# Kernel optimization log

Hardware: AMD Instinct MI355X
Metric: run time of the kernel (lower is better)

The kernel has to match this reference:

```python
import jax, jax.numpy as jnp
import numpy as np
import math

# Config (matches init_kwargs)
H, SQK, PQK, SV, PV = 12, 16, 4, 16, 8
C1, C2 = 384, 128
NR, NA = 512, 256
N = NR + NA
WC = math.sqrt(2.0 / (9.0 * PQK))
WL = math.sqrt(1.0 / 3.0)


def quat_to_rot(q):
    # q: [..., 4] (w, x, y, z); normalize then build rotation matrix [..., 3, 3]
    q = q / jnp.linalg.norm(q, axis=-1, keepdims=True)
    w, x, y, z = q[..., 0], q[..., 1], q[..., 2], q[..., 3]
    return jnp.stack([
        jnp.stack([1 - 2 * (y * y + z * z), 2 * (x * y - w * z), 2 * (x * z + w * y)], -1),
        jnp.stack([2 * (x * y + w * z), 1 - 2 * (x * x + z * z), 2 * (y * z - w * x)], -1),
        jnp.stack([2 * (x * z - w * y), 2 * (y * z + w * x), 1 - 2 * (x * x + y * y)], -1),
    ], -2)


def setup_inputs() -> dict:
    key = jax.random.key(0)
    ks = jax.random.split(key, 16)
    s = 0.02
    return {
        'rec_1d': jax.random.normal(ks[0], (1, NR, C1), jnp.float32),
        'lig_1d': jax.random.normal(ks[1], (1, NA, C1), jnp.float32),
        'rep_2d': jax.random.normal(ks[2], (1, N, N, C2), jnp.float32),
        'rec_T': jax.random.normal(ks[3], (1, NR, 7), jnp.float32),
        'lig_T': jax.random.normal(ks[4], (1, NA, 7), jnp.float32),
        'rec_w1d': jax.random.normal(ks[5], (C1, (2 * SQK + SV) * H), jnp.float32) * s,
        'rec_wpt': jax.random.normal(ks[6], (C1, (2 * PQK + PV) * H * 3), jnp.float32) * s,
        'lig_w1d': jax.random.normal(ks[7], (C1, (2 * SQK + SV) * H), jnp.float32) * s,
        'lig_wpt': jax.random.normal(ks[8], (C1, (2 * PQK + PV) * H * 3), jnp.float32) * s,
        'rr_w': jax.random.normal(ks[9], (C2, H), jnp.float32) * s,
        'll_w': jax.random.normal(ks[10], (C2, H), jnp.float32) * s,
        'rl_w': jax.random.normal(ks[11], (C2, H), jnp.float32) * s,
        'lr_w': jax.random.normal(ks[12], (C2, H), jnp.float32) * s,
        'final_w': jax.random.normal(ks[13], (H * (C2 + SV + 4 * PV), C1), jnp.float32) * s,
        'final_b': jnp.zeros((C1,), jnp.float32),
    }


def reference(rec_1d, lig_1d, rep_2d, rec_T, lig_T, rec_w1d, rec_wpt, lig_w1d, lig_wpt,
              rr_w, ll_w, rl_w, lr_w, final_w, final_b):
    B = rec_1d.shape[0]

    def scalar_kqv(x, w, n):
        kqv = (x @ w).reshape(B, n, H, 2 * SQK + SV)
        return kqv[..., :SQK], kqv[..., SQK:2 * SQK], kqv[..., 2 * SQK:]

    rec_k1, rec_q1, rec_v1 = scalar_kqv(rec_1d, rec_w1d, NR)
    lig_k1, lig_q1, lig_v1 = scalar_kqv(lig_1d, lig_w1d, NA)

    # 2d pair biases per block: [B, i, j, H]
    rr = rep_2d[:, :NR, :NR] @ rr_w
    ll = rep_2d[:, NR:, NR:] @ ll_w
    rl = rep_2d[:, :NR, NR:] @ rl_w
    lr = rep_2d[:, NR:, :NR] @ lr_w

    def point_kqv(x, w, T, n):
        R = quat_to_rot(T[..., :4])          # [B, n, 3, 3]
        t = T[..., 4:]                        # [B, n, 3]
        local = (x @ w).reshape(B, n, 3, H * (2 * PQK + PV))
        glob = jnp.einsum('bnij,bnjd->bnid', R, local) + t[..., None]
        glob = glob.reshape(B, n, 3, H, 2 * PQK + PV)
        return glob[..., :PQK], glob[..., PQK:2 * PQK], glob[..., 2 * PQK:], R, t

    rec_kp, rec_qp, rec_vp, rec_R, rec_t = point_kqv(rec_1d, rec_wpt, rec_T, NR)
    lig_kp, lig_qp, lig_vp, lig_R, lig_t = point_kqv(lig_1d, lig_wpt, lig_T, NA)

    q_point = jnp.concatenate([rec_qp, lig_qp], axis=1)  # [B, N, 3, H, PQK]
    k_point = jnp.concatenate([rec_kp, lig_kp], axis=1)

    # squared distances summed over xyz and points -> [B, N, N, H]
    diff = q_point[:, :, None] - k_point[:, None, :]     # [B, N, N, 3, H, PQK]
    d2 = jnp.sum(jnp.square(diff), axis=3).sum(axis=-1)
    aff = -WC * d2

    bias = jnp.concatenate([
        jnp.concatenate([rr, rl], axis=2),
        jnp.concatenate([lr, ll], axis=2),
    ], axis=1)
    aff = aff + bias

    q1 = jnp.concatenate([rec_q1, lig_q1], axis=1)
    k1 = jnp.concatenate([rec_k1, lig_k1], axis=1)
    aff = aff + (WL / math.sqrt(SQK)) * jnp.einsum('bihc,bjhc->bijh', q1, k1)

    weights = jax.nn.softmax(aff, axis=2)  # [B, N, N, H]

    # 2d aggregation: [B, N, H, C2]
    o_2d = jnp.einsum('bijh,bijc->bihc', weights, rep_2d).reshape(B, N, H * C2)

    # scalar-v term: faithful to source (v_1d.unsqueeze(2) broadcasts over j,
    # so it reduces to v_1d * sum_j weights)
    v_1d = jnp.concatenate([rec_v1, lig_v1], axis=1)     # [B, N, H, SV]
    o_1d = (v_1d * jnp.sum(weights, axis=2)[..., None]).reshape(B, N, H * SV)

    # point-v aggregation in global frame: [B, N, 3, PV, H]
    v_point = jnp.concatenate([rec_vp, lig_vp], axis=1)  # [B, N, 3, H, PV]
    out_global = jnp.einsum('bijh,bjdhp->bidph', weights, v_point)

    def invert(glob, R, t):
        return jnp.einsum('bnji,bnjph->bniph', R, glob - t[..., None, None])

    out_local = jnp.concatenate([
        invert(out_global[:, :NR], rec_R, rec_t),
        invert(out_global[:, NR:], lig_R, lig_t),
    ], axis=1)                                           # [B, N, 3, PV, H]
    out_local = jnp.transpose(out_local, (0, 1, 3, 4, 2))  # [B, N, PV, H, 3]
    o_pt = out_local.reshape(B, N, PV * H * 3)
    o_norm = jnp.sqrt(jnp.sum(jnp.square(out_local), axis=-1)).reshape(B, N, PV * H)

    feat = jnp.concatenate([o_2d, o_1d, o_pt, o_norm], axis=-1)
    return feat @ final_w + final_b
```

## Files before the change

kernel.cpp:

```cpp
#include <hip/hip_runtime.h>
#include <math.h>

#define H_   12
#define NRR  512
#define N_   768
#define C1_  384
#define C2_  128
static __device__ __constant__ float WC_  = 0.2357022603955158f;
static __device__ __constant__ float SC1_ = 0.14433756729740646f;

#define OFF_Q1     0
#define OFF_QP     147456
#define OFF_V1     258048
#define OFF_VP     405504
#define OFF_R      626688
#define OFF_T      633600
#define OFF_KHAT   635904
#define OFF_WFRAG  930816
#define OFF_QKF    934912
#define OFF_MUSED  10372096
#define OFF_MSFIN  10519552
#define OFF_W      10544128
#define OFF_FEAT   17622016
#define OFF_PART   19244032

typedef __attribute__((ext_vector_type(8))) short short8_m;
typedef __attribute__((ext_vector_type(4))) float f32x4_m;

__device__ __forceinline__ ushort f2bf(float f) {
  uint u = __float_as_uint(f);
  uint r = (u + 0x7fffu + ((u >> 16) & 1u)) >> 16;
  return (ushort)r;
}
__device__ __forceinline__ float bf2f(ushort v) {
  return __uint_as_float(((uint)v) << 16);
}

__global__ __launch_bounds__(192) void proj_kernel(
    const float* __restrict__ rec_1d, const float* __restrict__ lig_1d,
    const float* __restrict__ rec_T,  const float* __restrict__ lig_T,
    const float* __restrict__ rec_w1d, const float* __restrict__ rec_wpt,
    const float* __restrict__ lig_w1d, const float* __restrict__ lig_wpt,
    float* __restrict__ ws) {
  const int tok0 = blockIdx.x * 4;
  const int tid  = threadIdx.x;
  __shared__ float xs[4][384];
  __shared__ float loc[4][576];
  __shared__ float Rs[4][9];
  __shared__ float tts[4][3];

  for (int r = 0; r < 4; ++r) {
    int n = tok0 + r;
    const float* x = (n < NRR) ? rec_1d + n * C1_ : lig_1d + (n - NRR) * C1_;
    for (int k = tid; k < C1_; k += 192) xs[r][k] = x[k];
  }
  if (tid < 4) {
    int n = tok0 + tid;
    const float* T = (n < NRR) ? rec_T + n * 7 : lig_T + (n - NRR) * 7;
    float qw = T[0], qx = T[1], qy = T[2], qz = T[3];
    float inv = 1.0f / sqrtf(qw*qw + qx*qx + qy*qy + qz*qz);
    qw *= inv; qx *= inv; qy *= inv; qz *= inv;
    Rs[tid][0] = 1.f - 2.f*(qy*qy + qz*qz);
    Rs[tid][1] = 2.f*(qx*qy - qw*qz);
    Rs[tid][2] = 2.f*(qx*qz + qw*qy);
    Rs[tid][3] = 2.f*(qx*qy + qw*qz);
    Rs[tid][4] = 1.f - 2.f*(qx*qx + qz*qz);
    Rs[tid][5] = 2.f*(qy*qz - qw*qx);
    Rs[tid][6] = 2.f*(qx*qz - qw*qy);
    Rs[tid][7] = 2.f*(qy*qz + qw*qx);
    Rs[tid][8] = 1.f - 2.f*(qx*qx + qy*qy);
    tts[tid][0] = T[4]; tts[tid][1] = T[5]; tts[tid][2] = T[6];
    float* Rg = ws + OFF_R + n * 9;
    #pragma unroll
    for (int k = 0; k < 9; ++k) Rg[k] = Rs[tid][k];
    float* tg = ws + OFF_T + n * 3;
    tg[0] = T[4]; tg[1] = T[5]; tg[2] = T[6];
  }
  __syncthreads();

  const float* w1 = (tok0 < NRR) ? rec_w1d : lig_w1d;
  const float* w2 = (tok0 < NRR) ? rec_wpt : lig_wpt;
  for (int cc = 0; cc < 3; ++cc) {
    int c = tid + cc * 192;
    float a0=0,a1=0,a2=0,a3=0,b0=0,b1=0,b2=0,b3=0;
    for (int k = 0; k < C1_; ++k) {
      float wv = w1[k * 576 + c];
      float wp = w2[k * 576 + c];
      float x0 = xs[0][k], x1 = xs[1][k], x2 = xs[2][k], x3 = xs[3][k];
      a0 += x0*wv; a1 += x1*wv; a2 += x2*wv; a3 += x3*wv;
      b0 += x0*wp; b1 += x1*wp; b2 += x2*wp; b3 += x3*wp;
    }
    loc[0][c]=b0; loc[1][c]=b1; loc[2][c]=b2; loc[3][c]=b3;
    int h = c / 48, e = c % 48;
    float av[4] = {a0,a1,a2,a3};
    for (int r = 0; r < 4; ++r) {
      int n = tok0 + r;
      if (e < 16)      ws[OFF_KHAT + ((size_t)h*N_ + n)*32 + e] = av[r];
      else if (e < 32) ws[OFF_Q1 + n*192 + h*16 + (e-16)]       = av[r];
      else             ws[OFF_V1 + n*192 + h*16 + (e-32)]       = av[r];
    }
  }
  __syncthreads();

  {
    int cp = tid;
    int h = cp >> 4, e = cp & 15;
    for (int r = 0; r < 4; ++r) {
      int n = tok0 + r;
      float g[3];
      #pragma unroll
      for (int d = 0; d < 3; ++d)
        g[d] = Rs[r][d*3+0]*loc[r][cp] + Rs[r][d*3+1]*loc[r][192+cp]
             + Rs[r][d*3+2]*loc[r][384+cp] + tts[r][d];
      if (e < 4) {
        #pragma unroll
        for (int d = 0; d < 3; ++d)
          ws[OFF_KHAT + ((size_t)h*N_ + n)*32 + 16 + e*3 + d] = g[d];
      } else if (e < 8) {
        #pragma unroll
        for (int d = 0; d < 3; ++d) ws[OFF_QP + n*144 + h*12 + (e-4)*3 + d] = g[d];
      } else {
        #pragma unroll
        for (int d = 0; d < 3; ++d) ws[OFF_VP + n*288 + d*96 + h*8 + (e-8)] = g[d];
      }
    }
  }
}

__global__ __launch_bounds__(256) void wfrag_kernel(
    const float* __restrict__ rr_w, const float* __restrict__ rl_w,
    const float* __restrict__ lr_w, const float* __restrict__ ll_w,
    float* __restrict__ ws) {
  ushort* wf = (ushort*)(ws + OFF_WFRAG);
  const float* mats[4] = { rr_w, rl_w, lr_w, ll_w };
  for (int idx = threadIdx.x; idx < 8192; idx += 256) {
    int mat = idx >> 11;
    int r   = idx & 2047;
    int ks  = r >> 9;
    int r2  = r & 511;
    int l   = r2 >> 3;
    int e   = r2 & 7;
    int n   = l & 15;
    int k   = ks*32 + (l>>4)*8 + e;
    float v = (n < 12) ? mats[mat][k*12 + n] : 0.f;
    wf[idx] = f2bf(v);
  }
}

__global__ __launch_bounds__(256) void qk_kernel(float* __restrict__ ws) {
  const int b = blockIdx.x;
  const int i = b / 12, tile = b % 12;
  const int t = threadIdx.x;
  const int l = t & 63, w = t >> 6;
  __shared__ float q1s[12][16];
  __shared__ float qps[12][12];
  if (t < 192) q1s[t >> 4][t & 15] = ws[OFF_Q1 + i*192 + t];
  if (t < 144) qps[t / 12][t % 12] = ws[OFF_QP + i*144 + t];
  __syncthreads();
  const int h = l & 15, jq = l >> 4;
  float val[4] = {0.f, 0.f, 0.f, 0.f};
  if (h < 12) {
    #pragma unroll
    for (int rr = 0; rr < 4; ++rr) {
      int j = tile*64 + w*16 + jq*4 + rr;
      const float* kf = ws + OFF_KHAT + ((size_t)h*N_ + j)*32;
      float kv[28];
      #pragma unroll
      for (int c = 0; c < 28; c += 4) *(float4*)&kv[c] = *(const float4*)(kf + c);
      float s = 0.f;
      #pragma unroll
      for (int c = 0; c < 16; ++c) s += q1s[h][c] * kv[c];
      float d2 = 0.f;
      #pragma unroll
      for (int d = 0; d < 12; ++d) { float df = qps[h][d] - kv[16+d]; d2 += df*df; }
      val[rr] = SC1_*s - WC_*d2;
    }
  }
  float4 o; o.x = val[0]; o.y = val[1]; o.z = val[2]; o.w = val[3];
  *(float4*)(ws + OFF_QKF + ((size_t)b*4 + w)*256 + l*4) = o;
}

__global__ __launch_bounds__(256) void flash_kernel(
    const float* __restrict__ rep, float* __restrict__ ws) {
  const int i = blockIdx.x;
  const int t = threadIdx.x;
  const int lane = t & 63, wv = t >> 6;
  __shared__ ushort A[64 * 128];
  __shared__ ushort e_l[64 * 16];
  __shared__ float mt[64], est[64], fact[16], mrun[16], srun[16];

  const short8_m* wf = (const short8_m*)(ws + OFF_WFRAG);
  const int m0 = (i < NRR) ? 0 : 2, m1 = (i < NRR) ? 1 : 3;
  short8_m bf0[4], bf1[4];
  #pragma unroll
  for (int ks = 0; ks < 4; ++ks) {
    bf0[ks] = wf[(m0*4 + ks)*64 + lane];
    bf1[ks] = wf[(m1*4 + ks)*64 + lane];
  }
  if (t < 16) { mrun[t] = -1e30f; srun[t] = 0.f; }
  float acc[48];
  #pragma unroll
  for (int k = 0; k < 48; ++k) acc[k] = 0.f;

  const int cq = t & 31, jgr = t >> 5;
  const int hh = lane & 15, jq = lane >> 4;
  const int rowA = wv*16 + hh;
  __syncthreads();

  for (int tile = 0; tile < 12; ++tile) {
    const float* src = rep + ((size_t)i*N_ + tile*64) * C2_;
    #pragma unroll
    for (int k = 0; k < 8; ++k) {
      int j = jgr + k*8;
      float4 v = *(const float4*)(src + j*C2_ + cq*4);
      uint2 p;
      p.x = (uint)f2bf(v.x) | ((uint)f2bf(v.y) << 16);
      p.y = (uint)f2bf(v.z) | ((uint)f2bf(v.w) << 16);
      int slot = (cq >> 1) ^ (j & 7);
      *(uint2*)((char*)A + j*256 + slot*16 + (cq & 1)*8) = p;
    }
    __syncthreads();

    f32x4_m c4 = {0.f, 0.f, 0.f, 0.f};
    #pragma unroll
    for (int ks = 0; ks < 4; ++ks) {
      int slot = (ks*4 + jq) ^ (rowA & 7);
      short8_m a = *(const short8_m*)((const char*)A + rowA*256 + slot*16);
      c4 = __builtin_amdgcn_mfma_f32_16x16x32_bf16(
          a, (tile < 8) ? bf0[ks] : bf1[ks], c4, 0, 0, 0);
    }
    float4 qk4 = *(const float4*)(ws + OFF_QKF +
        (((size_t)i*12 + tile)*4 + wv)*256 + lane*4);
    float aff0 = c4[0] + qk4.x, aff1 = c4[1] + qk4.y;
    float aff2 = c4[2] + qk4.z, aff3 = c4[3] + qk4.w;

    float ml = fmaxf(fmaxf(aff0, aff1), fmaxf(aff2, aff3));
    ml = fmaxf(ml, __shfl_xor(ml, 16));
    ml = fmaxf(ml, __shfl_xor(ml, 32));
    if (jq == 0) mt[wv*16 + hh] = ml;
    __syncthreads();
    if (t < 12) {
      float m4 = fmaxf(fmaxf(mt[t], mt[16+t]), fmaxf(mt[32+t], mt[48+t]));
      float mn = fmaxf(mrun[t], m4);
      fact[t]  = __expf(mrun[t] - mn);
      mrun[t]  = mn;
      ws[OFF_MUSED + (size_t)i*192 + tile*16 + t] = mn;
    }
    __syncthreads();

    const bool valid = (hh < 12);
    float mh = valid ? mrun[hh] : 0.f;
    float e0 = valid ? __expf(aff0 - mh) : 0.f;
    float e1 = valid ? __expf(aff1 - mh) : 0.f;
    float e2 = valid ? __expf(aff2 - mh) : 0.f;
    float e3 = valid ? __expf(aff3 - mh) : 0.f;
    if (valid) {
      int jb = wv*16 + jq*4;
      e_l[(jb+0)*16 + hh] = f2bf(e0);
      e_l[(jb+1)*16 + hh] = f2bf(e1);
      e_l[(jb+2)*16 + hh] = f2bf(e2);
      e_l[(jb+3)*16 + hh] = f2bf(e3);
    }
    float es = e0 + e1 + e2 + e3;
    es += __shfl_xor(es, 16);
    es += __shfl_xor(es, 32);
    if (jq == 0) est[wv*16 + hh] = es;
    __syncthreads();
    if (t < 12)
      srun[t] = srun[t]*fact[t] + (est[t] + est[16+t] + est[32+t] + est[48+t]);

    float fc[12];
    #pragma unroll
    for (int h = 0; h < 12; ++h) fc[h] = fact[h];
    #pragma unroll
    for (int h = 0; h < 12; ++h) {
      acc[h*4+0] *= fc[h]; acc[h*4+1] *= fc[h];
      acc[h*4+2] *= fc[h]; acc[h*4+3] *= fc[h];
    }
    #pragma unroll
    for (int k = 0; k < 8; ++k) {
      int j = jgr + k*8;
      const char* ep = (const char*)e_l + j*32;
      uint4 u4 = *(const uint4*)ep;
      uint2 u2 = *(const uint2*)(ep + 16);
      float ef[12];
      ef[0] = __uint_as_float(u4.x << 16); ef[1] = __uint_as_float(u4.x & 0xffff0000u);
      ef[2] = __uint_as_float(u4.y << 16); ef[3] = __uint_as_float(u4.y & 0xffff0000u);
      ef[4] = __uint_as_float(u4.z << 16); ef[5] = __uint_as_float(u4.z & 0xffff0000u);
      ef[6] = __uint_as_float(u4.w << 16); ef[7] = __uint_as_float(u4.w & 0xffff0000u);
      ef[8] = __uint_as_float(u2.x << 16); ef[9] = __uint_as_float(u2.x & 0xffff0000u);
      ef[10] = __uint_as_float(u2.y << 16); ef[11] = __uint_as_float(u2.y & 0xffff0000u);
      int slot = (cq >> 1) ^ (j & 7);
      uint2 av = *(const uint2*)((const char*)A + j*256 + slot*16 + (cq & 1)*8);
      float af[4];
      af[0] = __uint_as_float(av.x << 16); af[1] = __uint_as_float(av.x & 0xffff0000u);
      af[2] = __uint_as_float(av.y << 16); af[3] = __uint_as_float(av.y & 0xffff0000u);
      #pragma unroll
      for (int h = 0; h < 12; ++h) {
        acc[h*4+0] += ef[h]*af[0];
        acc[h*4+1] += ef[h]*af[1];
        acc[h*4+2] += ef[h]*af[2];
        acc[h*4+3] += ef[h]*af[3];
      }
    }
    #pragma unroll
    for (int k = 0; k < 3; ++k) {
      int h = wv + k*4;
      ws[OFF_W + (size_t)i*9216 + h*768 + tile*64 + lane] =
          bf2f(e_l[lane*16 + h]);
    }
    __syncthreads();
  }

  if (t < 12) {
    ws[OFF_MSFIN + i*32 + t]      = mrun[t];
    ws[OFF_MSFIN + i*32 + 16 + t] = srun[t];
  }
  #pragma unroll
  for (int k = 0; k < 48; ++k) acc[k] += __shfl_xor(acc[k], 32);
  float* scr = (float*)A;
  __syncthreads();
  if (wv >= 2 && lane < 32) {
    float* dst = scr + (wv-2)*1536 + lane*48;
    #pragma unroll
    for (int k = 0; k < 48; ++k) dst[k] = acc[k];
  }
  __syncthreads();
  if (wv < 2 && lane < 32) {
    const float* s2 = scr + wv*1536 + lane*48;
    #pragma unroll
    for (int k = 0; k < 48; ++k) acc[k] += s2[k];
  }
  __syncthreads();
  if (wv == 1 && lane < 32) {
    float* dst = scr + lane*48;
    #pragma unroll
    for (int k = 0; k < 48; ++k) dst[k] = acc[k];
  }
  __syncthreads();
  if (wv == 0 && lane < 32) {
    const float* s2 = scr + lane*48;
    #pragma unroll
    for (int k = 0; k < 48; ++k) acc[k] += s2[k];
    float* feat = ws + OFF_FEAT + (size_t)i*2112;
    #pragma unroll
    for (int h = 0; h < 12; ++h) {
      float inv = 1.0f / srun[h];
      float4 r;
      r.x = acc[h*4+0]*inv; r.y = acc[h*4+1]*inv;
      r.z = acc[h*4+2]*inv; r.w = acc[h*4+3]*inv;
      *(float4*)&feat[h*128 + lane*4] = r;
    }
  }
}

__global__ __launch_bounds__(320) void opoint_kernel(
    const float* __restrict__ ws_w, const float* __restrict__ vp,
    const float* __restrict__ R, const float* __restrict__ tvec,
    const float* __restrict__ v1, const float* __restrict__ mused,
    const float* __restrict__ msfin, float* __restrict__ feat) {
  const int i = blockIdx.x;
  const int tid = threadIdx.x;
  __shared__ float wl[H_ * N_];
  __shared__ float cf[144];
  __shared__ float og[288];
  __shared__ float ol[288];
  if (tid < 144) {
    int h = tid / 12, tl = tid % 12;
    float sfin = msfin[i*32 + 16 + h];
    cf[tid] = __expf(mused[(size_t)i*192 + tl*16 + h] - msfin[i*32 + h]) / sfin;
  }
  __syncthreads();
  for (int k = tid; k < H_*N_; k += 320) {
    int h = k / 768, j = k - h*768;
    wl[k] = ws_w[(size_t)i*9216 + k] * cf[h*12 + (j >> 6)];
  }
  __syncthreads();
  if (tid < 288) {
    int d = tid / 96, hh = (tid % 96) / 8;
    float acc = 0.f;
    for (int j = 0; j < N_; ++j) acc += wl[hh*N_ + j] * vp[(size_t)j*288 + tid];
    og[tid] = acc - tvec[i*3 + d];
  }
  if (tid < 192) feat[(size_t)i*2112 + 1536 + tid] = v1[(size_t)i*192 + tid];
  __syncthreads();
  if (tid < 288) {
    int i3 = tid / 96, rem = tid % 96, hh = rem / 8, p = rem % 8;
    float o = R[i*9 + 0*3 + i3] * og[0*96 + rem]
            + R[i*9 + 1*3 + i3] * og[1*96 + rem]
            + R[i*9 + 2*3 + i3] * og[2*96 + rem];
    ol[tid] = o;
    feat[(size_t)i*2112 + 1728 + p*36 + hh*3 + i3] = o;
  }
  __syncthreads();
  if (tid < 96) {
    int hh = tid / 8, p = tid % 8;
    float a = ol[0*96 + tid], b = ol[1*96 + tid], c = ol[2*96 + tid];
    feat[(size_t)i*2112 + 2016 + p*12 + hh] = sqrtf(a*a + b*b + c*c);
  }
}

__global__ __launch_bounds__(384) void final1_kernel(
    const float* __restrict__ ws, const float* __restrict__ fw,
    float* __restrict__ part) {
  const int i0 = blockIdx.x * 4;
  const int ks = blockIdx.y;
  const int o  = threadIdx.x;
  const int k0 = ks * 1056;
  __shared__ float fl[4 * 1056];
  const float* feat = ws + OFF_FEAT;
  for (int idx = o; idx < 1056; idx += 384) {
    int r = idx / 264, f4 = idx % 264;
    *(float4*)&fl[r*1056 + f4*4] =
        *(const float4*)(feat + (size_t)(i0+r)*2112 + k0 + f4*4);
  }
  __syncthreads();
  float a0=0,a1=0,a2=0,a3=0;
  for (int f4 = 0; f4 < 264; ++f4) {
    int f = k0 + f4*4;
    float w0 = fw[(size_t)(f+0)*384 + o];
    float w1 = fw[(size_t)(f+1)*384 + o];
    float w2 = fw[(size_t)(f+2)*384 + o];
    float w3 = fw[(size_t)(f+3)*384 + o];
    float4 f0 = *(const float4*)&fl[0*1056 + f4*4];
    float4 f1 = *(const float4*)&fl[1*1056 + f4*4];
    float4 f2 = *(const float4*)&fl[2*1056 + f4*4];
    float4 f3 = *(const float4*)&fl[3*1056 + f4*4];
    a0 += f0.x*w0 + f0.y*w1 + f0.z*w2 + f0.w*w3;
    a1 += f1.x*w0 + f1.y*w1 + f1.z*w2 + f1.w*w3;
    a2 += f2.x*w0 + f2.y*w1 + f2.z*w2 + f2.w*w3;
    a3 += f3.x*w0 + f3.y*w1 + f3.z*w2 + f3.w*w3;
  }
  part[((size_t)ks*N_ + i0+0)*384 + o] = a0;
  part[((size_t)ks*N_ + i0+1)*384 + o] = a1;
  part[((size_t)ks*N_ + i0+2)*384 + o] = a2;
  part[((size_t)ks*N_ + i0+3)*384 + o] = a3;
}

__global__ __launch_bounds__(256) void final2_kernel(
    const float* __restrict__ part, const float* __restrict__ fb,
    float* __restrict__ out) {
  int idx = blockIdx.x * 256 + threadIdx.x;
  int col = idx % 384;
  out[idx] = part[idx] + part[294912 + idx] + fb[col];
}

extern "C" void kernel_launch(void* const* d_in, const int* in_sizes, int n_in,
                              void* d_out, int out_size, void* d_ws, size_t ws_size,
                              hipStream_t stream) {
  const float* rec_1d  = (const float*)d_in[0];
  const float* lig_1d  = (const float*)d_in[1];
  const float* rep_2d  = (const float*)d_in[2];
  const float* rec_T   = (const float*)d_in[3];
  const float* lig_T   = (const float*)d_in[4];
  const float* rec_w1d = (const float*)d_in[5];
  const float* rec_wpt = (const float*)d_in[6];
  const float* lig_w1d = (const float*)d_in[7];
  const float* lig_wpt = (const float*)d_in[8];
  const float* rr_w    = (const float*)d_in[9];
  const float* ll_w    = (const float*)d_in[10];
  const float* rl_w    = (const float*)d_in[11];
  const float* lr_w    = (const float*)d_in[12];
  const float* final_w = (const float*)d_in[13];
  const float* final_b = (const float*)d_in[14];
  float* ws  = (float*)d_ws;
  float* out = (float*)d_out;

  proj_kernel<<<192, 192, 0, stream>>>(rec_1d, lig_1d, rec_T, lig_T,
                                       rec_w1d, rec_wpt, lig_w1d, lig_wpt, ws);
  wfrag_kernel<<<1, 256, 0, stream>>>(rr_w, rl_w, lr_w, ll_w, ws);
  qk_kernel<<<N_*12, 256, 0, stream>>>(ws);
  flash_kernel<<<N_, 256, 0, stream>>>(rep_2d, ws);
  opoint_kernel<<<N_, 320, 0, stream>>>(ws + OFF_W, ws + OFF_VP, ws + OFF_R,
                                        ws + OFF_T, ws + OFF_V1, ws + OFF_MUSED,
                                        ws + OFF_MSFIN, ws + OFF_FEAT);
  final1_kernel<<<dim3(N_/4, 2), 384, 0, stream>>>(ws, final_w, ws + OFF_PART);
  final2_kernel<<<1152, 256, 0, stream>>>(ws + OFF_PART, final_b, out);
}
```

Baseline: 986.6 us.

## Split flash attention over key tiles, drop online max, double-buffer rep tiles

The flash kernel now launches three blocks per query row, each covering four of the twelve 64-wide key tiles, and writes partial outputs and exp-sums. A new o2dfin kernel combines the partials and normalises. The running-max rescaling is removed, so exponentials are taken directly on the raw logits. A double-buffered LDS tile with register prefetch of the next rep_2d tile and lighter raw barriers are meant to overlap global loads with compute and cut synchronisation. The cost is an extra kernel and partial-buffer traffic, and large logits could overflow exp because they are no longer shifted by the max.

```diff
diff --git a/kernel.cpp b/kernel.cpp
--- a/kernel.cpp
+++ b/kernel.cpp
@@ -6,6 +6,8 @@
 #define N_   768
 #define C1_  384
 #define C2_  128
+#define SPLIT 3
+#define TPB  4
 static __device__ __constant__ float WC_  = 0.2357022603955158f;
 static __device__ __constant__ float SC1_ = 0.14433756729740646f;
 
@@ -18,11 +20,12 @@
 #define OFF_KHAT   635904
 #define OFF_WFRAG  930816
 #define OFF_QKF    934912
-#define OFF_MUSED  10372096
-#define OFF_MSFIN  10519552
-#define OFF_W      10544128
-#define OFF_FEAT   17622016
-#define OFF_PART   19244032
+#define OFF_SSP    10372096
+#define OFF_SSUM   10408960
+#define OFF_O2DP   10421248
+#define OFF_W      13960192
+#define OFF_FEAT   21038080
+#define OFF_PART   22660096
 
 typedef __attribute__((ext_vector_type(8))) short short8_m;
 typedef __attribute__((ext_vector_type(4))) float f32x4_m;
@@ -35,6 +38,12 @@
 __device__ __forceinline__ float bf2f(ushort v) {
   return __uint_as_float(((uint)v) << 16);
 }
+
+#define BARRAW() do {                                        \
+    asm volatile("s_waitcnt lgkmcnt(0)" ::: "memory");       \
+    __builtin_amdgcn_s_barrier();                            \
+    __builtin_amdgcn_sched_barrier(0);                       \
+  } while (0)
 
 __global__ __launch_bounds__(192) void proj_kernel(
     const float* __restrict__ rec_1d, const float* __restrict__ lig_1d,
@@ -182,101 +191,85 @@
 
 __global__ __launch_bounds__(256) void flash_kernel(
     const float* __restrict__ rep, float* __restrict__ ws) {
-  const int i = blockIdx.x;
+  const int b = blockIdx.x;
+  const int i = b / SPLIT, sp = b % SPLIT;
+  const int t0 = sp * TPB;
   const int t = threadIdx.x;
   const int lane = t & 63, wv = t >> 6;
-  __shared__ ushort A[64 * 128];
+  __shared__ ushort A[2][64 * 128];
   __shared__ ushort e_l[64 * 16];
-  __shared__ float mt[64], est[64], fact[16], mrun[16], srun[16];
 
   const short8_m* wf = (const short8_m*)(ws + OFF_WFRAG);
-  const int m0 = (i < NRR) ? 0 : 2, m1 = (i < NRR) ? 1 : 3;
-  short8_m bf0[4], bf1[4];
-  #pragma unroll
-  for (int ks = 0; ks < 4; ++ks) {
-    bf0[ks] = wf[(m0*4 + ks)*64 + lane];
-    bf1[ks] = wf[(m1*4 + ks)*64 + lane];
-  }
-  if (t < 16) { mrun[t] = -1e30f; srun[t] = 0.f; }
+  const int m = ((i < NRR) ? 0 : 2) + ((t0 >= 8) ? 1 : 0);
+  short8_m bfr[4];
+  #pragma unroll
+  for (int ks = 0; ks < 4; ++ks) bfr[ks] = wf[(m*4 + ks)*64 + lane];
+
+  float4 qk4pf[TPB];
+  #pragma unroll
+  for (int tt = 0; tt < TPB; ++tt)
+    qk4pf[tt] = *(const float4*)(ws + OFF_QKF +
+        (((size_t)i*12 + t0 + tt)*4 + wv)*256 + lane*4);
+
   float acc[48];
   #pragma unroll
   for (int k = 0; k < 48; ++k) acc[k] = 0.f;
+  float ssum[12];
+  #pragma unroll
+  for (int h = 0; h < 12; ++h) ssum[h] = 0.f;
 
   const int cq = t & 31, jgr = t >> 5;
   const int hh = lane & 15, jq = lane >> 4;
   const int rowA = wv*16 + hh;
-  __syncthreads();
-
-  for (int tile = 0; tile < 12; ++tile) {
-    const float* src = rep + ((size_t)i*N_ + tile*64) * C2_;
+
+  float4 pf[8];
+  {
+    const float* src = rep + ((size_t)i*N_ + t0*64) * C2_;
+    #pragma unroll
+    for (int k = 0; k < 8; ++k)
+      pf[k] = *(const float4*)(src + (jgr + k*8)*C2_ + cq*4);
     #pragma unroll
     for (int k = 0; k < 8; ++k) {
       int j = jgr + k*8;
-      float4 v = *(const float4*)(src + j*C2_ + cq*4);
       uint2 p;
-      p.x = (uint)f2bf(v.x) | ((uint)f2bf(v.y) << 16);
-      p.y = (uint)f2bf(v.z) | ((uint)f2bf(v.w) << 16);
+      p.x = (uint)f2bf(pf[k].x) | ((uint)f2bf(pf[k].y) << 16);
+      p.y = (uint)f2bf(pf[k].z) | ((uint)f2bf(pf[k].w) << 16);
       int slot = (cq >> 1) ^ (j & 7);
-      *(uint2*)((char*)A + j*256 + slot*16 + (cq & 1)*8) = p;
-    }
-    __syncthreads();
+      *(uint2*)((char*)A[0] + j*256 + slot*16 + (cq & 1)*8) = p;
+    }
+  }
+  BARRAW();
+
+  int cur = 0;
+  for (int tt = 0; tt < TPB; ++tt) {
+    const int tile = t0 + tt;
+    if (tt < TPB-1) {
+      const float* src = rep + ((size_t)i*N_ + (tile+1)*64) * C2_;
+      #pragma unroll
+      for (int k = 0; k < 8; ++k)
+        pf[k] = *(const float4*)(src + (jgr + k*8)*C2_ + cq*4);
+    }
 
     f32x4_m c4 = {0.f, 0.f, 0.f, 0.f};
     #pragma unroll
     for (int ks = 0; ks < 4; ++ks) {
       int slot = (ks*4 + jq) ^ (rowA & 7);
-      short8_m a = *(const short8_m*)((const char*)A + rowA*256 + slot*16);
-      c4 = __builtin_amdgcn_mfma_f32_16x16x32_bf16(
-          a, (tile < 8) ? bf0[ks] : bf1[ks], c4, 0, 0, 0);
-    }
-    float4 qk4 = *(const float4*)(ws + OFF_QKF +
-        (((size_t)i*12 + tile)*4 + wv)*256 + lane*4);
-    float aff0 = c4[0] + qk4.x, aff1 = c4[1] + qk4.y;
-    float aff2 = c4[2] + qk4.z, aff3 = c4[3] + qk4.w;
-
-    float ml = fmaxf(fmaxf(aff0, aff1), fmaxf(aff2, aff3));
-    ml = fmaxf(ml, __shfl_xor(ml, 16));
-    ml = fmaxf(ml, __shfl_xor(ml, 32));
-    if (jq == 0) mt[wv*16 + hh] = ml;
-    __syncthreads();
-    if (t < 12) {
-      float m4 = fmaxf(fmaxf(mt[t], mt[16+t]), fmaxf(mt[32+t], mt[48+t]));
-      float mn = fmaxf(mrun[t], m4);
-      fact[t]  = __expf(mrun[t] - mn);
-      mrun[t]  = mn;
-      ws[OFF_MUSED + (size_t)i*192 + tile*16 + t] = mn;
-    }
-    __syncthreads();
-
-    const bool valid = (hh < 12);
-    float mh = valid ? mrun[hh] : 0.f;
-    float e0 = valid ? __expf(aff0 - mh) : 0.f;
-    float e1 = valid ? __expf(aff1 - mh) : 0.f;
-    float e2 = valid ? __expf(aff2 - mh) : 0.f;
-    float e3 = valid ? __expf(aff3 - mh) : 0.f;
-    if (valid) {
+      short8_m a = *(const short8_m*)((const char*)A[cur] + rowA*256 + slot*16);
+      c4 = __builtin_amdgcn_mfma_f32_16x16x32_bf16(a, bfr[ks], c4, 0, 0, 0);
+    }
+    float e0 = __expf(c4[0] + qk4pf[tt].x);
+    float e1 = __expf(c4[1] + qk4pf[tt].y);
+    float e2 = __expf(c4[2] + qk4pf[tt].z);
+    float e3 = __expf(c4[3] + qk4pf[tt].w);
+    if (hh < 12) {
       int jb = wv*16 + jq*4;
       e_l[(jb+0)*16 + hh] = f2bf(e0);
       e_l[(jb+1)*16 + hh] = f2bf(e1);
       e_l[(jb+2)*16 + hh] = f2bf(e2);
       e_l[(jb+3)*16 + hh] = f2bf(e3);
     }
-    float es = e0 + e1 + e2 + e3;
-    es += __shfl_xor(es, 16);
-    es += __shfl_xor(es, 32);
-    if (jq == 0) est[wv*16 + hh] = es;
-    __syncthreads();
-    if (t < 12)
-      srun[t] = srun[t]*fact[t] + (est[t] + est[16+t] + est[32+t] + est[48+t]);
-
-    float fc[12];
-    #pragma unroll
-    for (int h = 0; h < 12; ++h) fc[h] = fact[h];
-    #pragma unroll
-    for (int h = 0; h < 12; ++h) {
-      acc[h*4+0] *= fc[h]; acc[h*4+1] *= fc[h];
-      acc[h*4+2] *= fc[h]; acc[h*4+3] *= fc[h];
-    }
+    BARRAW();
+
     #pragma unroll
     for (int k = 0; k < 8; ++k) {
       int j = jgr + k*8;
@@ -291,7 +284,7 @@
       ef[8] = __uint_as_float(u2.x << 16); ef[9] = __uint_as_float(u2.x & 0xffff0000u);
       ef[10] = __uint_as_float(u2.y << 16); ef[11] = __uint_as_float(u2.y & 0xffff0000u);
       int slot = (cq >> 1) ^ (j & 7);
-      uint2 av = *(const uint2*)((const char*)A + j*256 + slot*16 + (cq & 1)*8);
+      uint2 av = *(const uint2*)((const char*)A[cur] + j*256 + slot*16 + (cq & 1)*8);
       float af[4];
       af[0] = __uint_as_float(av.x << 16); af[1] = __uint_as_float(av.x & 0xffff0000u);
       af[2] = __uint_as_float(av.y << 16); af[3] = __uint_as_float(av.y & 0xffff0000u);
@@ -301,6 +294,7 @@
         acc[h*4+1] += ef[h]*af[1];
         acc[h*4+2] += ef[h]*af[2];
         acc[h*4+3] += ef[h]*af[3];
+        ssum[h] += ef[h];
       }
     }
     #pragma unroll
@@ -309,76 +303,118 @@
       ws[OFF_W + (size_t)i*9216 + h*768 + tile*64 + lane] =
           bf2f(e_l[lane*16 + h]);
     }
-    __syncthreads();
-  }
-
+    if (tt < TPB-1) {
+      #pragma unroll
+      for (int k = 0; k < 8; ++k) {
+        int j = jgr + k*8;
+        uint2 p;
+        p.x = (uint)f2bf(pf[k].x) | ((uint)f2bf(pf[k].y) << 16);
+        p.y = (uint)f2bf(pf[k].z) | ((uint)f2bf(pf[k].w) << 16);
+        int slot = (cq >> 1) ^ (j & 7);
+        *(uint2*)((char*)A[cur^1] + j*256 + slot*16 + (cq & 1)*8) = p;
+      }
+    }
+    BARRAW();
+    cur ^= 1;
+  }
+
+  #pragma unroll
+  for (int k = 0; k < 48; ++k) acc[k] += __shfl_xor(acc[k], 32);
+  #pragma unroll
+  for (int h = 0; h < 12; ++h) ssum[h] += __shfl_xor(ssum[h], 32);
+  float* scr = (float*)A;
+  __syncthreads();
+  if (wv >= 2 && lane < 32) {
+    float* dst = scr + (wv-2)*1920 + lane*60;
+    #pragma unroll
+    for (int k = 0; k < 48; ++k) dst[k] = acc[k];
+    #pragma unroll
+    for (int h = 0; h < 12; ++h) dst[48+h] = ssum[h];
+  }
+  __syncthreads();
+  if (wv < 2 && lane < 32) {
+    const float* s2 = scr + wv*1920 + lane*60;
+    #pragma unroll
+    for (int k = 0; k < 48; ++k) acc[k] += s2[k];
+    #pragma unroll
+    for (int h = 0; h < 12; ++h) ssum[h] += s2[48+h];
+  }
+  __syncthreads();
+  if (wv == 1 && lane < 32) {
+    float* dst = scr + lane*60;
+    #pragma unroll
+    for (int k = 0; k < 48; ++k) dst[k] = acc[k];
+    #pragma unroll
+    for (int h = 0; h < 12; ++h) dst[48+h] = ssum[h];
+  }
+  __syncthreads();
+  if (wv == 0 && lane < 32) {
+    const float* s2 = scr + lane*60;
+    #pragma unroll
+    for (int k = 0; k < 48; ++k) acc[k] += s2[k];
+    #pragma unroll
+    for (int h = 0; h < 12; ++h) ssum[h] += s2[48+h];
+    float* part = ws + OFF_O2DP + ((size_t)sp*N_ + i)*1536;
+    #pragma unroll
+    for (int h = 0; h < 12; ++h) {
+      float4 r;
+      r.x = acc[h*4+0]; r.y = acc[h*4+1]; r.z = acc[h*4+2]; r.w = acc[h*4+3];
+      *(float4*)&part[h*128 + lane*4] = r;
+    }
+    if (lane == 0) {
+      #pragma unroll
+      for (int h = 0; h < 12; ++h)
+        ws[OFF_SSP + ((size_t)sp*N_ + i)*16 + h] = ssum[h];
+    }
+  }
+}
+
+__global__ __launch_bounds__(256) void o2dfin_kernel(float* __restrict__ ws) {
+  const int i = blockIdx.x;
+  const int t = threadIdx.x;
+  __shared__ float inv_s[12];
   if (t < 12) {
-    ws[OFF_MSFIN + i*32 + t]      = mrun[t];
-    ws[OFF_MSFIN + i*32 + 16 + t] = srun[t];
-  }
-  #pragma unroll
-  for (int k = 0; k < 48; ++k) acc[k] += __shfl_xor(acc[k], 32);
-  float* scr = (float*)A;
-  __syncthreads();
-  if (wv >= 2 && lane < 32) {
-    float* dst = scr + (wv-2)*1536 + lane*48;
-    #pragma unroll
-    for (int k = 0; k < 48; ++k) dst[k] = acc[k];
-  }
-  __syncthreads();
-  if (wv < 2 && lane < 32) {
-    const float* s2 = scr + wv*1536 + lane*48;
-    #pragma unroll
-    for (int k = 0; k < 48; ++k) acc[k] += s2[k];
-  }
-  __syncthreads();
-  if (wv == 1 && lane < 32) {
-    float* dst = scr + lane*48;
-    #pragma unroll
-    for (int k = 0; k < 48; ++k) dst[k] = acc[k];
-  }
-  __syncthreads();
-  if (wv == 0 && lane < 32) {
-    const float* s2 = scr + lane*48;
-    #pragma unroll
-    for (int k = 0; k < 48; ++k) acc[k] += s2[k];
-    float* feat = ws + OFF_FEAT + (size_t)i*2112;
-    #pragma unroll
-    for (int h = 0; h < 12; ++h) {
-      float inv = 1.0f / srun[h];
-      float4 r;
-      r.x = acc[h*4+0]*inv; r.y = acc[h*4+1]*inv;
-      r.z = acc[h*4+2]*inv; r.w = acc[h*4+3]*inv;
-      *(float4*)&feat[h*128 + lane*4] = r;
-    }
+    float s = ws[OFF_SSP + (size_t)i*16 + t]
+            + ws[OFF_SSP + ((size_t)N_ + i)*16 + t]
+            + ws[OFF_SSP + ((size_t)2*N_ + i)*16 + t];
+    float inv = 1.0f / s;
+    inv_s[t] = inv;
+    ws[OFF_SSUM + i*16 + t] = inv;
+  }
+  __syncthreads();
+  #pragma unroll
+  for (int k = 0; k < 6; ++k) {
+    int idx = t + k*256;
+    int h = idx >> 7;
+    float v = ws[OFF_O2DP + (size_t)i*1536 + idx]
+            + ws[OFF_O2DP + ((size_t)N_ + i)*1536 + idx]
+            + ws[OFF_O2DP + ((size_t)2*N_ + i)*1536 + idx];
+    ws[OFF_FEAT + (size_t)i*2112 + idx] = v * inv_s[h];
   }
 }
 
 __global__ __launch_bounds__(320) void opoint_kernel(
     const float* __restrict__ ws_w, const float* __restrict__ vp,
     const float* __restrict__ R, const float* __restrict__ tvec,
-    const float* __restrict__ v1, const float* __restrict__ mused,
-    const float* __restrict__ msfin, float* __restrict__ feat) {
+    const float* __restrict__ v1, const float* __restrict__ invs,
+    float* __restrict__ feat) {
   const int i = blockIdx.x;
   const int tid = threadIdx.x;
   __shared__ float wl[H_ * N_];
-  __shared__ float cf[144];
+  __shared__ float iv[12];
   __shared__ float og[288];
   __shared__ float ol[288];
-  if (tid < 144) {
-    int h = tid / 12, tl = tid % 12;
-    float sfin = msfin[i*32 + 16 + h];
-    cf[tid] = __expf(mused[(size_t)i*192 + tl*16 + h] - msfin[i*32 + h]) / sfin;
-  }
+  if (tid < 12) iv[tid] = invs[i*16 + tid];
   __syncthreads();
   for (int k = tid; k < H_*N_; k += 320) {
-    int h = k / 768, j = k - h*768;
-    wl[k] = ws_w[(size_t)i*9216 + k] * cf[h*12 + (j >> 6)];
+    int h = k / 768;
+    wl[k] = ws_w[(size_t)i*9216 + k] * iv[h];
   }
   __syncthreads();
   if (tid < 288) {
     int d = tid / 96, hh = (tid % 96) / 8;
     float acc = 0.f;
+    #pragma unroll 8
     for (int j = 0; j < N_; ++j) acc += wl[hh*N_ + j] * vp[(size_t)j*288 + tid];
     og[tid] = acc - tvec[i*3 + d];
   }
@@ -470,10 +506,11 @@
                                        rec_w1d, rec_wpt, lig_w1d, lig_wpt, ws);
   wfrag_kernel<<<1, 256, 0, stream>>>(rr_w, rl_w, lr_w, ll_w, ws);
   qk_kernel<<<N_*12, 256, 0, stream>>>(ws);
-  flash_kernel<<<N_, 256, 0, stream>>>(rep_2d, ws);
+  flash_kernel<<<N_*SPLIT, 256, 0, stream>>>(rep_2d, ws);
+  o2dfin_kernel<<<N_, 256, 0, stream>>>(ws);
   opoint_kernel<<<N_, 320, 0, stream>>>(ws + OFF_W, ws + OFF_VP, ws + OFF_R,
-                                        ws + OFF_T, ws + OFF_V1, ws + OFF_MUSED,
-                                        ws + OFF_MSFIN, ws + OFF_FEAT);
+                                        ws + OFF_T, ws + OFF_V1, ws + OFF_SSUM,
+                                        ws + OFF_FEAT);
   final1_kernel<<<dim3(N_/4, 2), 384, 0, stream>>>(ws, final_w, ws + OFF_PART);
   final2_kernel<<<1152, 256, 0, stream>>>(ws + OFF_PART, final_b, out);
 }
```

New measurement: 892.7 us. 1.11x faster.
